# Performance work log

Hardware: AMD Instinct MI355X
Metric: run time of the kernel (lower is better)

The kernel has to match this reference:

```python
import math
import jax, jax.numpy as jnp
import numpy as np

LOW_FREQ = 1
FACTOR = 1


def setup_inputs() -> dict:
    key = jax.random.key(0)
    x = jax.random.normal(key, (8, 4096, 512), dtype=jnp.float32)
    return {"x": x}


def reference(x):
    b, t, d = x.shape
    x_freq = jnp.fft.rfft(x, axis=1)  # (b, t//2+1, d) complex
    if t % 2 == 0:
        x_freq = x_freq[:, LOW_FREQ:-1]
        f = jnp.fft.rfftfreq(t)[LOW_FREQ:-1]
    else:
        x_freq = x_freq[:, LOW_FREQ:]
        f = jnp.fft.rfftfreq(t)[LOW_FREQ:]
    length = x_freq.shape[1]
    top_k = int(FACTOR * math.log(length))

    # top-k |X(f)| independently per (batch, channel)
    amp_all = jnp.abs(x_freq)                      # (b, F, d)
    _, idx = jax.lax.top_k(jnp.transpose(amp_all, (0, 2, 1)), top_k)  # (b, d, k)
    idx = jnp.transpose(idx, (0, 2, 1))            # (b, k, d)
    x_sel = jnp.take_along_axis(x_freq, idx, axis=1)  # (b, k, d) complex
    f_sel = f[idx].astype(jnp.float32)             # (b, k, d)

    # extrapolate: append conjugate components with negated frequency
    x2 = jnp.concatenate([x_sel, jnp.conj(x_sel)], axis=1)  # (b, 2k, d)
    f2 = jnp.concatenate([f_sel, -f_sel], axis=1)           # (b, 2k, d)
    amp = jnp.abs(x2)[:, :, None, :]               # (b, 2k, 1, d)
    phase = jnp.angle(x2)[:, :, None, :]           # (b, 2k, 1, d)
    tt = jnp.arange(t, dtype=jnp.float32)[None, None, :, None]  # (1,1,t,1)
    x_time = amp * jnp.cos(2.0 * math.pi * f2[:, :, None, :] * tt + phase)  # (b,2k,t,d)
    return jnp.sum(x_time, axis=1)                 # (b, t, d)
```

## Files before the change

kernel.cpp:

```cpp
#include <hip/hip_runtime.h>
#include <math.h>

#define B 8
#define T 4096
#define D 512
#define NPAIR ((B * D) / 2)
#define TOPK 7
#define PAD(e) ((e) + ((e) >> 4) + ((e) >> 8))

__device__ __forceinline__ int drev(int k) {
  return ((k & 15) << 8) | (k & 240) | (k >> 8);
}
__device__ __forceinline__ int pdrev(int k) {
  const int e = drev(k);
  return PAD(e);
}

__device__ __forceinline__ float2 cmul(float2 a, float2 b) {
  return make_float2(a.x * b.x - a.y * b.y, a.x * b.y + a.y * b.x);
}
__device__ __forceinline__ float2 cadd(float2 a, float2 b) { return make_float2(a.x + b.x, a.y + b.y); }
__device__ __forceinline__ float2 csub(float2 a, float2 b) { return make_float2(a.x - b.x, a.y - b.y); }
__device__ __forceinline__ float2 cmul_negi(float2 a) { return make_float2(a.y, -a.x); }

__device__ __forceinline__ unsigned long long shfl_xor_u64(unsigned long long v, int off) {
  const unsigned lo = __shfl_xor((unsigned)v, off);
  const unsigned hi = __shfl_xor((unsigned)(v >> 32), off);
  return ((unsigned long long)hi << 32) | lo;
}
__device__ __forceinline__ unsigned long long umax64(unsigned long long a, unsigned long long b) {
  return (a > b) ? a : b;
}

__device__ __forceinline__ void dft4(float2& a, float2& b, float2& c, float2& d) {
  const float2 t0 = cadd(a, c), t1 = csub(a, c);
  const float2 t2 = cadd(b, d), t3n = cmul_negi(csub(b, d));
  a = cadd(t0, t2);
  b = cadd(t1, t3n);
  c = csub(t0, t2);
  d = csub(t1, t3n);
}

#define C16 0.92387953251f
#define S16 0.38268343236f
#define RS2 0.70710678119f
__device__ __forceinline__ void dft16(float2 r[16]) {
  dft4(r[0], r[4], r[8],  r[12]);
  dft4(r[1], r[5], r[9],  r[13]);
  dft4(r[2], r[6], r[10], r[14]);
  dft4(r[3], r[7], r[11], r[15]);
  const float2 W1 = make_float2(C16, -S16);
  const float2 W2 = make_float2(RS2, -RS2);
  const float2 W3 = make_float2(S16, -C16);
  const float2 W6 = make_float2(-RS2, -RS2);
  const float2 W9 = make_float2(-C16, S16);
  r[5]  = cmul(r[5],  W1);
  r[9]  = cmul(r[9],  W2);
  r[13] = cmul(r[13], W3);
  r[6]  = cmul(r[6],  W2);
  r[10] = cmul_negi(r[10]);
  r[14] = cmul(r[14], W6);
  r[7]  = cmul(r[7],  W3);
  r[11] = cmul(r[11], W6);
  r[15] = cmul(r[15], W9);
  dft4(r[0],  r[1],  r[2],  r[3]);
  dft4(r[4],  r[5],  r[6],  r[7]);
  dft4(r[8],  r[9],  r[10], r[11]);
  dft4(r[12], r[13], r[14], r[15]);
}
#define SW4(k) ((((k) & 3) << 2) | ((k) >> 2))

__device__ __forceinline__ void twiddle_tree(float2 w, float2 tw[16]) {
  tw[1] = w;
  tw[2] = cmul(w, w);
  tw[3] = cmul(tw[1], tw[2]);
  tw[4] = cmul(tw[2], tw[2]);
  tw[5] = cmul(tw[1], tw[4]);
  tw[6] = cmul(tw[2], tw[4]);
  tw[7] = cmul(tw[3], tw[4]);
  tw[8] = cmul(tw[4], tw[4]);
  tw[9]  = cmul(tw[1], tw[8]);
  tw[10] = cmul(tw[2], tw[8]);
  tw[11] = cmul(tw[3], tw[8]);
  tw[12] = cmul(tw[4], tw[8]);
  tw[13] = cmul(tw[5], tw[8]);
  tw[14] = cmul(tw[6], tw[8]);
  tw[15] = cmul(tw[7], tw[8]);
}

__global__ __launch_bounds__(256) void k_transpose_pack(const float* __restrict__ x,
                                                        float2* __restrict__ xp) {
  __shared__ float tT[64][65];
  const int b  = blockIdx.z;
  const int t0 = blockIdx.x * 64;
  const int d0 = blockIdx.y * 64;
  const int tid = threadIdx.x;

  const int c4 = tid & 15;
  const int r0 = tid >> 4;
  for (int r = r0; r < 64; r += 16) {
    const float4 v = *(const float4*)&x[((size_t)b * T + (t0 + r)) * D + d0 + 4 * c4];
    tT[4 * c4 + 0][r] = v.x;
    tT[4 * c4 + 1][r] = v.y;
    tT[4 * c4 + 2][r] = v.z;
    tT[4 * c4 + 3][r] = v.w;
  }
  __syncthreads();

  const int tt  = tid & 31;
  const int rp0 = tid >> 5;
  for (int rp = rp0; rp < 32; rp += 8) {
    const float2 a  = *(const float2*)&tT[2 * rp][2 * tt];
    const float2 bb = *(const float2*)&tT[2 * rp + 1][2 * tt];
    const float4 o = make_float4(a.x, bb.x, a.y, bb.y);
    *(float4*)&xp[((size_t)b * (D / 2) + (d0 / 2 + rp)) * T + t0 + 2 * tt] = o;
  }
}

__global__ __launch_bounds__(256) void k_fft_topk(float2* __restrict__ xp) {
  __shared__ float2 Z[PAD(T - 1) + 1];
  __shared__ unsigned long long s_cand[2][2][8];

  const int tid  = threadIdx.x;
  const int lane = tid & 63;
  const int wid  = tid >> 6;
  float2* g = xp + (size_t)blockIdx.x * T;

  float2 r[16];
  #pragma unroll
  for (int g4 = 0; g4 < 4; ++g4) {
    #pragma unroll
    for (int a = 0; a < 4; ++a) {
      const int idx = g4 + 4 * a;
      r[idx] = g[(idx << 8) + tid];
    }
  }

  dft16(r);
  {
    float s, c;
    __sincosf(6.283185307179586f / 4096.0f * (float)tid, &s, &c);
    float2 tw[16];
    twiddle_tree(make_float2(c, -s), tw);
    const int pa = tid + (tid >> 4);
    Z[pa] = r[0];
    #pragma unroll
    for (int k1 = 1; k1 < 16; ++k1) Z[pa + 273 * k1] = cmul(r[SW4(k1)], tw[k1]);
  }
  __syncthreads();

  {
    const int m1  = tid & 15;
    const int pb  = 273 * (tid >> 4) + m1;
    #pragma unroll
    for (int m2 = 0; m2 < 16; ++m2) r[m2] = Z[pb + 17 * m2];
    dft16(r);
    float s, c;
    __sincosf(6.283185307179586f / 256.0f * (float)m1, &s, &c);
    float2 tw[16];
    twiddle_tree(make_float2(c, -s), tw);
    Z[pb] = r[0];
    #pragma unroll
    for (int p = 1; p < 16; ++p) Z[pb + 17 * p] = cmul(r[SW4(p)], tw[p]);
  }
  __syncthreads();

  {
    const int pc = 17 * tid + (tid >> 4);
    #pragma unroll
    for (int m1 = 0; m1 < 16; ++m1) r[m1] = Z[pc + m1];
    dft16(r);
    #pragma unroll
    for (int q = 0; q < 16; ++q) Z[pc + q] = r[SW4(q)];
  }
  __syncthreads();

  const int sh = wid >> 1;
  const int u  = ((wid & 1) << 6) | lane;
  const int Bk0 = pdrev(1 + u);
  const int Bk1 = pdrev(1 + u + 128);
  const int Bn0 = pdrev(4095 - u);
  const int Bn1 = pdrev(4095 - u - 128);
  unsigned long long key[16];
  #pragma unroll
  for (int j = 0; j < 16; ++j) {
    const int ek = ((j & 1) ? Bk1 : Bk0) + (j >> 1);
    const int en = ((j & 1) ? Bn1 : Bn0) - (j >> 1);
    const float2 zk = Z[ek];
    const float2 zn = Z[en];
    float re, im;
    if (sh == 0) { re = zk.x + zn.x; im = zk.y - zn.y; }
    else         { re = zk.y + zn.y; im = zn.x - zk.x; }
    const float a = re * re + im * im;
    const int k = 1 + u + (j << 7);
    key[j] = ((unsigned long long)(__float_as_uint(a) | 0x80000000u) << 32)
           | (unsigned)(0xFFFFu ^ k);
  }
  if (u == 127) key[15] = 0ull;

  #pragma unroll
  for (int it = 0; it < TOPK; ++it) {
    unsigned long long ma = key[0], mb = key[8];
    #pragma unroll
    for (int j = 1; j < 8; ++j) {
      ma = umax64(ma, key[j]);
      mb = umax64(mb, key[8 + j]);
    }
    unsigned long long m = umax64(ma, mb);
    #pragma unroll
    for (int off = 1; off < 64; off <<= 1) {
      const unsigned long long o = shfl_xor_u64(m, off);
      m = umax64(m, o);
    }
    #pragma unroll
    for (int j = 0; j < 16; ++j)
      if (key[j] == m) key[j] = 0ull;
    if (lane == 0) s_cand[sh][wid & 1][it] = m;
  }
  __syncthreads();

  if ((wid & 1) == 0) {
    const int sh2 = wid >> 1;
    const int w   = (lane >> 3) & 1;
    const int i   = lane & 7;
    unsigned long long kk =
        (lane < 16 && i < TOPK) ? s_cand[sh2][w][i] : 0ull;
    #pragma unroll
    for (int ksz = 2; ksz <= 16; ksz <<= 1) {
      #pragma unroll
      for (int j = ksz >> 1; j > 0; j >>= 1) {
        const unsigned long long o = shfl_xor_u64(kk, j);
        const bool dirDesc = ((lane & ksz) == 0);
        const bool lower   = ((lane & j) == 0);
        const unsigned long long big = (kk > o) ? kk : o;
        const unsigned long long sml = (kk > o) ? o : kk;
        kk = (lower == dirDesc) ? big : sml;
      }
    }
    if (lane < TOPK) {
      const int k = 0xFFFF ^ (int)(kk & 0xFFFFull);
      const float2 zk = Z[pdrev(k)];
      const float2 zn = Z[pdrev(T - k)];
      float re, im;
      if (sh2 == 0) { re = 0.5f * (zk.x + zn.x); im = 0.5f * (zk.y - zn.y); }
      else          { re = 0.5f * (zk.y + zn.y); im = 0.5f * (zn.x - zk.x); }
      ((float4*)g)[sh2 * TOPK + lane] = make_float4((float)k, re, im, 0.0f);
    }
  }
}

__global__ __launch_bounds__(256) void k_eval(const float* __restrict__ ws,
                                              float* __restrict__ out) {
  __shared__ float  tile[64][64];
  __shared__ float4 s_coef[64 * TOPK];

  const int tid = threadIdx.x;
  const int b   = blockIdx.z;
  const int d0  = blockIdx.y * 64;
  const int t0  = blockIdx.x * 64;

  for (int idx = tid; idx < 64 * TOPK; idx += 256) {
    const int s = idx / TOPK, j = idx - s * TOPK;
    const int P = (b * D + d0) / 2 + (s >> 1);
    const int sh = s & 1;
    s_coef[idx] = ((const float4*)(ws + (size_t)P * (2 * T)))[sh * TOPK + j];
  }
  __syncthreads();

  const int dl = tid & 63;
  const int tg = tid >> 6;
  const float w0 = 6.283185307179586f / 4096.0f;

  float re[TOPK], im[TOPK], cc[TOPK], ss[TOPK], cd[TOPK], sd[TOPK];
  const int ts = t0 + tg;
  #pragma unroll
  for (int j = 0; j < TOPK; ++j) {
    const float4 v = s_coef[dl * TOPK + j];
    const int k = (int)v.x;
    re[j] = 2.0f * v.y;
    im[j] = 2.0f * v.z;
    const float a0 = w0 * (float)((k * ts) & (T - 1));
    const float ad = w0 * (float)((4 * k) & (T - 1));
    ss[j] = __sinf(a0); cc[j] = __cosf(a0);
    sd[j] = __sinf(ad); cd[j] = __cosf(ad);
  }

  #pragma unroll
  for (int i = 0; i < 16; ++i) {
    float acc = 0.0f;
    #pragma unroll
    for (int j = 0; j < TOPK; ++j) {
      acc += re[j] * cc[j] - im[j] * ss[j];
      const float nc = cc[j] * cd[j] - ss[j] * sd[j];
      const float ns = ss[j] * cd[j] + cc[j] * sd[j];
      cc[j] = nc; ss[j] = ns;
    }
    tile[tg + 4 * i][dl] = acc;
  }
  __syncthreads();

  const int c4 = tid & 15;
  const int rw = tid >> 4;
  for (int rr = rw; rr < 64; rr += 16) {
    const float4 v = *(const float4*)&tile[rr][4 * c4];
    *(float4*)&out[((size_t)b * T + (t0 + rr)) * D + d0 + 4 * c4] = v;
  }
}

extern "C" void kernel_launch(void* const* d_in, const int* in_sizes, int n_in,
                              void* d_out, int out_size, void* d_ws, size_t ws_size,
                              hipStream_t stream) {
  const float* x = (const float*)d_in[0];
  float* out = (float*)d_out;
  float2* xp = (float2*)d_ws;

  dim3 tgrid(T / 64, D / 64, B);
  hipLaunchKernelGGL(k_transpose_pack, tgrid, dim3(256), 0, stream, x, xp);
  hipLaunchKernelGGL(k_fft_topk, dim3(NPAIR), dim3(256), 0, stream, xp);
  hipLaunchKernelGGL(k_eval, tgrid, dim3(256), 0, stream, (const float*)d_ws, out);
}
```

Baseline: 173.1 us.

## Fuse first FFT radix-16 stage into transpose-pack kernel

The transpose/pack kernel now also performs the first radix-16 DFT pass with twiddles. It loads strided time rows into shared memory, runs the butterfly and writes the partially transformed data to the workspace. The FFT kernel then starts from the second stage, dropping one shared-memory pass and one barrier per block. The cost is more work and a different tiling in the first kernel (16x16 grid with 32-column tiles). The global write pattern also changes and may coalesce less well.

Result: no change. 172.9 us (-0.1%).

```diff
diff --git a/kernel.cpp b/kernel.cpp
--- a/kernel.cpp
+++ b/kernel.cpp
@@ -88,32 +88,59 @@
   tw[15] = cmul(tw[7], tw[8]);
 }
 
-__global__ __launch_bounds__(256) void k_transpose_pack(const float* __restrict__ x,
-                                                        float2* __restrict__ xp) {
-  __shared__ float tT[64][65];
-  const int b  = blockIdx.z;
-  const int t0 = blockIdx.x * 64;
-  const int d0 = blockIdx.y * 64;
+__global__ __launch_bounds__(256) void k_fftA(const float* __restrict__ x,
+                                              float2* __restrict__ xp) {
+  __shared__ float2 S[4368];
+
   const int tid = threadIdx.x;
-
-  const int c4 = tid & 15;
-  const int r0 = tid >> 4;
-  for (int r = r0; r < 64; r += 16) {
-    const float4 v = *(const float4*)&x[((size_t)b * T + (t0 + r)) * D + d0 + 4 * c4];
-    tT[4 * c4 + 0][r] = v.x;
-    tT[4 * c4 + 1][r] = v.y;
-    tT[4 * c4 + 2][r] = v.z;
-    tT[4 * c4 + 3][r] = v.w;
-  }
-  __syncthreads();
-
-  const int tt  = tid & 31;
-  const int rp0 = tid >> 5;
-  for (int rp = rp0; rp < 32; rp += 8) {
-    const float2 a  = *(const float2*)&tT[2 * rp][2 * tt];
-    const float2 bb = *(const float2*)&tT[2 * rp + 1][2 * tt];
-    const float4 o = make_float4(a.x, bb.x, a.y, bb.y);
-    *(float4*)&xp[((size_t)b * (D / 2) + (d0 / 2 + rp)) * T + t0 + 2 * tt] = o;
+  const int mt  = blockIdx.x;
+  const int dt  = blockIdx.y;
+  const int b   = blockIdx.z;
+
+  {
+    float* tile = (float*)S;
+    const int l  = tid & 7;
+    const int rb = tid >> 3;
+    #pragma unroll
+    for (int pass = 0; pass < 8; ++pass) {
+      const int r = rb + (pass << 5);
+      const int a = r >> 4, mi = r & 15;
+      const int t = (mt << 4) + mi + (a << 8);
+      const float4 v = *(const float4*)&x[((size_t)b * T + t) * D + (dt << 5) + (l << 2)];
+      *(float4*)&tile[(r << 5) + (l << 2)] = v;
+    }
+  }
+  __syncthreads();
+
+  float2 r[16];
+  const int p  = tid & 15;
+  const int mi = tid >> 4;
+  #pragma unroll
+  for (int a = 0; a < 16; ++a)
+    r[a] = S[((a << 4) + mi) * 16 + p];
+  __syncthreads();
+  dft16(r);
+  {
+    const int m = (mt << 4) + mi;
+    float s, c;
+    __sincosf(6.283185307179586f / 4096.0f * (float)m, &s, &c);
+    float2 tw[16];
+    twiddle_tree(make_float2(c, -s), tw);
+    const int pe = 17 * p + mi;
+    S[pe] = r[0];
+    #pragma unroll
+    for (int k1 = 1; k1 < 16; ++k1) S[pe + 272 * k1] = cmul(r[SW4(k1)], tw[k1]);
+  }
+  __syncthreads();
+
+  {
+    const int sp = tid >> 4;
+    const int sm = tid & 15;
+    float2* gp = xp + ((size_t)b * (D / 2) + (dt << 4) + sp) * T + (mt << 4) + sm;
+    const int rbase = 17 * sp + sm;
+    #pragma unroll
+    for (int k1 = 0; k1 < 16; ++k1)
+      gp[k1 << 8] = S[rbase + 272 * k1];
   }
 }
 
@@ -127,48 +154,30 @@
   float2* g = xp + (size_t)blockIdx.x * T;
 
   float2 r[16];
-  #pragma unroll
-  for (int g4 = 0; g4 < 4; ++g4) {
-    #pragma unroll
-    for (int a = 0; a < 4; ++a) {
-      const int idx = g4 + 4 * a;
-      r[idx] = g[(idx << 8) + tid];
-    }
-  }
-
+  const int k1 = tid >> 4;
+  const int m1 = tid & 15;
+  {
+    const float2* gsrc = g + (k1 << 8) + m1;
+    #pragma unroll
+    for (int m2 = 0; m2 < 16; ++m2) r[m2] = gsrc[m2 << 4];
+  }
   dft16(r);
   {
-    float s, c;
-    __sincosf(6.283185307179586f / 4096.0f * (float)tid, &s, &c);
-    float2 tw[16];
-    twiddle_tree(make_float2(c, -s), tw);
-    const int pa = tid + (tid >> 4);
-    Z[pa] = r[0];
-    #pragma unroll
-    for (int k1 = 1; k1 < 16; ++k1) Z[pa + 273 * k1] = cmul(r[SW4(k1)], tw[k1]);
-  }
-  __syncthreads();
-
-  {
-    const int m1  = tid & 15;
-    const int pb  = 273 * (tid >> 4) + m1;
-    #pragma unroll
-    for (int m2 = 0; m2 < 16; ++m2) r[m2] = Z[pb + 17 * m2];
-    dft16(r);
     float s, c;
     __sincosf(6.283185307179586f / 256.0f * (float)m1, &s, &c);
     float2 tw[16];
     twiddle_tree(make_float2(c, -s), tw);
+    const int pb = 273 * k1 + m1;
     Z[pb] = r[0];
     #pragma unroll
-    for (int p = 1; p < 16; ++p) Z[pb + 17 * p] = cmul(r[SW4(p)], tw[p]);
+    for (int pp = 1; pp < 16; ++pp) Z[pb + 17 * pp] = cmul(r[SW4(pp)], tw[pp]);
   }
   __syncthreads();
 
   {
     const int pc = 17 * tid + (tid >> 4);
     #pragma unroll
-    for (int m1 = 0; m1 < 16; ++m1) r[m1] = Z[pc + m1];
+    for (int mm = 0; mm < 16; ++mm) r[mm] = Z[pc + mm];
     dft16(r);
     #pragma unroll
     for (int q = 0; q < 16; ++q) Z[pc + q] = r[SW4(q)];
@@ -314,8 +323,8 @@
   float* out = (float*)d_out;
   float2* xp = (float2*)d_ws;
 
-  dim3 tgrid(T / 64, D / 64, B);
-  hipLaunchKernelGGL(k_transpose_pack, tgrid, dim3(256), 0, stream, x, xp);
+  hipLaunchKernelGGL(k_fftA, dim3(16, 16, B), dim3(256), 0, stream, x, xp);
   hipLaunchKernelGGL(k_fft_topk, dim3(NPAIR), dim3(256), 0, stream, xp);
-  hipLaunchKernelGGL(k_eval, tgrid, dim3(256), 0, stream, (const float*)d_ws, out);
-}
+  hipLaunchKernelGGL(k_eval, dim3(T / 64, D / 64, B), dim3(256), 0, stream,
+                     (const float*)d_ws, out);
+}
```
